# Performance work log

Hardware: AMD Instinct MI355X
Metric: run time of the kernel (lower is better)

Reference implementation:

```python
import jax, jax.numpy as jnp
import numpy as np

B, CIN, CE, CA, N, S = 2, 64, 128, 128, 1024, 32
SCALE = np.sqrt(np.float32(CA))  # scale_mode == 'dimfts'


def _vnlin(W, x):
    # VNLinear: linear map over the channel dim of (B, C, 3, N, S)
    return jnp.einsum('oc,bcdns->bodns', W, x)


def setup_inputs() -> dict:
    key = jax.random.key(0)
    ks = jax.random.split(key, 16)
    def w(k, o, i):
        return (jax.random.normal(k, (o, i), jnp.float32) / np.sqrt(np.float32(i)))
    return {
        'group_xyz': jax.random.normal(ks[0], (B, N, S, 3), jnp.float32),
        'group_fts': jax.random.normal(ks[1], (B, CIN, 3, N, S), jnp.float32),
        'query_xyz': jax.random.normal(ks[2], (B, N, 3), jnp.float32),
        'W_e1': w(ks[3], CE, CIN), 'W_e2': w(ks[4], CE, CE),
        'W_q': w(ks[5], CA, CE), 'W_k': w(ks[6], CA, CE), 'W_v': w(ks[7], CA, CE),
        'W_r1': w(ks[8], 64, 1), 'W_r2': w(ks[9], CA, 64),
        'W_std': w(ks[10], 3, CA),
        'W_f1': w(ks[11], CA, CA * 3), 'b_f1': jax.random.normal(ks[12], (CA,), jnp.float32) * 0.02,
        'W_f2': w(ks[13], CA, CA), 'b_f2': jax.random.normal(ks[14], (CA,), jnp.float32) * 0.02,
    }


def reference(group_xyz, group_fts, query_xyz, W_e1, W_e2, W_q, W_k, W_v,
              W_r1, W_r2, W_std, W_f1, b_f1, W_f2, b_f2):
    # vnn_e: two stacked VNLinear layers
    group_emb = _vnlin(W_e2, _vnlin(W_e1, group_fts))        # (B, CE, 3, N, S)
    query_emb = group_emb[..., :1]                           # (B, CE, 3, N, 1)
    q = _vnlin(W_q, query_emb)                               # (B, CA, 3, N, 1)
    k = _vnlin(W_k, group_emb)                               # (B, CA, 3, N, S)
    v = _vnlin(W_v, group_emb)                               # (B, CA, 3, N, S)

    # positional relation: xyz_rel -> (B, 1, 3, N, S) -> vnn_r
    xyz_rel = group_xyz - query_xyz[:, :, None, :]           # (B, N, S, 3)
    xyz_rel = jnp.transpose(xyz_rel[:, :, :, None, :], (0, 3, 4, 1, 2))  # (B,1,3,N,S)
    pos_rel = _vnlin(W_r2, _vnlin(W_r1, xyz_rel))            # (B, CA, 3, N, S)

    # relation_func == 'sub'
    attn = q - k + pos_rel                                   # (B, CA, 3, N, S)

    # VNStdFeatureLin (dim=5, no frame normalization): z0 = VNLinear(CA->3)
    z0 = _vnlin(W_std, attn)                                 # (B, 3, 3, N, S)
    attn = jnp.einsum('bijns,bjkns->bikns', attn, z0)        # (B, CA, 3, N, S) invariant

    # attn_fwd: 1x1 conv -> ReLU -> 1x1 conv on (B, CA*3, N, S)
    attn = attn.reshape(B, CA * 3, N, S)
    h = jax.nn.relu(jnp.einsum('oc,bcns->bons', W_f1, attn) + b_f1[:, None, None])
    a = jnp.einsum('oc,bcns->bons', W_f2, h) + b_f2[:, None, None]  # (B, CA, N, S)

    a = jax.nn.softmax(a[:, :, None, :, :] / SCALE, axis=-1)  # (B, CA, 1, N, S)
    v = v + pos_rel
    resi = jnp.sum(a * v, axis=-1)                            # (B, CA, 3, N)
    return resi
```

## Files before the change

kernel.cpp:

```cpp
#include <hip/hip_runtime.h>
#include <hip/hip_bf16.h>
#include <math.h>

typedef __hip_bfloat16  bf16;
typedef __hip_bfloat162 bf162;
typedef __attribute__((ext_vector_type(8))) short short8;
typedef __attribute__((ext_vector_type(4))) float f32x4;

#define BB   2
#define CINC 64
#define NN   1024
#define SSS  32
#define NS   (NN * SSS)

#define OFF_QT   0
#define OFF_WR   8192
#define OFF_WE21 8320
#define OFF_KB   16512
#define OFF_VB   20608
#define OFF_F1B  24704
#define OFF_F2B  49280
#define WS_NEED_FLOATS 57472

#define S_ATT_B 0
#define S_FTS_B 26112
#define S_SCR_B 26112
#define S_Q_B   39936
#define S_XYZ_B 40704
#define SMEM_BYTES 40896

__device__ __forceinline__ float bf2f(short s) {
    unsigned int u = ((unsigned int)(unsigned short)s) << 16;
    return __uint_as_float(u);
}
__device__ __forceinline__ short f2bf(float f) {
    bf16 h = __float2bfloat16(f);
    return *reinterpret_cast<short*>(&h);
}
__device__ __forceinline__ unsigned pk2(float a, float b) {
    bf162 p = __float22bfloat162_rn(make_float2(a, b));
    return *reinterpret_cast<unsigned*>(&p);
}

__global__ __launch_bounds__(256) void prep1(const float* __restrict__ We1,
                                             const float* __restrict__ We2,
                                             float* __restrict__ ws) {
    int e = blockIdx.x * 256 + threadIdx.x;
    int o = e >> 6, c = e & 63;
    float acc = 0.f;
    for (int m = 0; m < 128; ++m)
        acc = fmaf(We2[o * 128 + m], We1[m * 64 + c], acc);
    ws[OFF_WE21 + o * 64 + c] = acc;
}

__global__ __launch_bounds__(256) void prep2(const float* __restrict__ Wq,
                                             const float* __restrict__ Wk,
                                             const float* __restrict__ Wv,
                                             const float* __restrict__ Wr1,
                                             const float* __restrict__ Wr2,
                                             const float* __restrict__ Wf1,
                                             const float* __restrict__ Wf2,
                                             float* __restrict__ ws) {
    const float* we21 = ws + OFF_WE21;
    int e = blockIdx.x * 256 + threadIdx.x;
    if (e < 8192) {
        int i = e >> 6, c = e & 63;
        float acc = 0.f;
        for (int o = 0; o < 128; ++o)
            acc = fmaf(Wq[i * 128 + o], we21[o * 64 + c], acc);
        ws[OFF_QT + c * 128 + i] = acc;
    } else if (e < 24576) {
        int le = e - 8192;
        const float* W = (le < 8192) ? Wk : Wv;
        bf16* dst = (bf16*)(ws + ((le < 8192) ? OFF_KB : OFF_VB));
        int li = le & 8191;
        int i = li >> 6, c = li & 63;
        float acc = 0.f;
        for (int o = 0; o < 128; ++o)
            acc = fmaf(W[i * 128 + o], we21[o * 64 + c], acc);
        dst[i * 64 + c] = __float2bfloat16(acc);
    } else if (e < 24704) {
        int i = e - 24576;
        float acc = 0.f;
        for (int m = 0; m < 64; ++m)
            acc = fmaf(Wr2[i * 64 + m], Wr1[m], acc);
        ws[OFF_WR + i] = acc;
    } else if (e < 24704 + 49152) {
        int f = e - 24704;
        int o = f / 384, kp = f - o * 384;
        int c = (kp & 127) * 3 + (kp >> 7);
        ((bf16*)(ws + OFF_F1B))[f] = __float2bfloat16(Wf1[o * 384 + c]);
    } else if (e < 24704 + 49152 + 16384) {
        int f = e - (24704 + 49152);
        ((bf16*)(ws + OFF_F2B))[f] = __float2bfloat16(Wf2[f]);
    }
}

__global__ __launch_bounds__(256, 2) void fused_main(
        const float* __restrict__ gxyz, const float* __restrict__ gfts,
        const float* __restrict__ qxyz, const float* __restrict__ Wstd,
        const float* __restrict__ bf1,  const float* __restrict__ bf2,
        const float* __restrict__ ws,   float* __restrict__ out) {
    extern __shared__ char smc[];
    short* s_att  = (short*)(smc + S_ATT_B);
    short* h_t    = s_att;
    short* a_t    = s_att + 4352;
    short* fts_s  = (short*)(smc + S_FTS_B);
    float* s_scr  = (float*)(smc + S_SCR_B);
    short* s_qh   = (short*)(smc + S_Q_B);
    short* s_xyzh = (short*)(smc + S_XYZ_B);

    const int t    = threadIdx.x;
    const int bid  = blockIdx.x;
    const int b    = bid >> 10;
    const int n    = bid & 1023;
    const int w    = t >> 6;
    const int lane = t & 63;
    const int quad = lane >> 4;
    const int lq   = lane & 15;
    const int wb   = 32 * w;

    const float* gb = gfts + (size_t)b * (CINC * 3 * NS) + n * SSS;

    for (int l4 = t; l4 < 1536; l4 += 256) {
        int c  = l4 / 24;
        int m4 = (l4 - c * 24) * 4;
        int d  = m4 >> 5, s = m4 & 31;
        float4 f = *(const float4*)(gb + (c * 3 + d) * NS + s);
        fts_s[(m4 + 0) * 72 + c] = f2bf(f.x);
        fts_s[(m4 + 1) * 72 + c] = f2bf(f.y);
        fts_s[(m4 + 2) * 72 + c] = f2bf(f.z);
        fts_s[(m4 + 3) * 72 + c] = f2bf(f.w);
    }
    if (t >= 160) {
        int id = t - 160;
        int d = id >> 5, s = id & 31;
        s_xyzh[id] = f2bf(gxyz[((b * NN + n) * SSS + s) * 3 + d]
                          - qxyz[(b * NN + n) * 3 + d]);
    }
    __syncthreads();

    if (t < 128) {
        const float* qtw = ws + OFF_QT;
        float q0 = 0.f, q1 = 0.f, q2 = 0.f;
        for (int c = 0; c < 64; ++c) {
            float wq = qtw[c * 128 + t];
            q0 = fmaf(wq, bf2f(fts_s[c]),           q0);
            q1 = fmaf(wq, bf2f(fts_s[32 * 72 + c]), q1);
            q2 = fmaf(wq, bf2f(fts_s[64 * 72 + c]), q2);
        }
        s_qh[t * 3 + 0] = f2bf(q0);
        s_qh[t * 3 + 1] = f2bf(q1);
        s_qh[t * 3 + 2] = f2bf(q2);
    }
    __syncthreads();

    f32x4 va[6][2];
    {
        const short* kb = (const short*)(ws + OFF_KB);
        const short* vb = (const short*)(ws + OFF_VB);
        short8 Bk[2][2], Bv[2][2];
        #pragma unroll
        for (int it = 0; it < 2; ++it) {
            int irow = (wb + it * 16 + lq) * 64 + quad * 8;
            Bk[it][0] = *(const short8*)(kb + irow);
            Bk[it][1] = *(const short8*)(kb + irow + 32);
            Bv[it][0] = *(const short8*)(vb + irow);
            Bv[it][1] = *(const short8*)(vb + irow + 32);
        }
        float wr2[2] = { ws[OFF_WR + wb + lq], ws[OFF_WR + wb + 16 + lq] };
        #pragma unroll
        for (int mt = 0; mt < 6; ++mt) {
            const short* ap = fts_s + (mt * 16 + lq) * 72 + quad * 8;
            short8 A0 = *(const short8*)(ap);
            short8 A1 = *(const short8*)(ap + 32);
            int d = mt >> 1;
            #pragma unroll
            for (int it = 0; it < 2; ++it) {
                f32x4 kk = {0.f, 0.f, 0.f, 0.f};
                kk = __builtin_amdgcn_mfma_f32_16x16x32_bf16(A0, Bk[it][0], kk, 0, 0, 0);
                kk = __builtin_amdgcn_mfma_f32_16x16x32_bf16(A1, Bk[it][1], kk, 0, 0, 0);
                f32x4 vv = {0.f, 0.f, 0.f, 0.f};
                vv = __builtin_amdgcn_mfma_f32_16x16x32_bf16(A0, Bv[it][0], vv, 0, 0, 0);
                vv = __builtin_amdgcn_mfma_f32_16x16x32_bf16(A1, Bv[it][1], vv, 0, 0, 0);
                int i = wb + it * 16 + lq;
                float qd = bf2f(s_qh[i * 3 + d]);
                #pragma unroll
                for (int reg = 0; reg < 4; ++reg) {
                    int m = mt * 16 + quad * 4 + reg;
                    float pos = wr2[it] * bf2f(s_xyzh[m]);
                    s_att[m * 136 + i] = f2bf(qd - kk[reg] + pos);
                    va[mt][it][reg] = vv[reg] + pos;
                }
            }
        }
    }
    __syncthreads();

    {
        short8 As[4];
        #pragma unroll
        for (int kc = 0; kc < 4; ++kc) {
            short8 a = {0, 0, 0, 0, 0, 0, 0, 0};
            if (lq < 3) {
                const float* wp = Wstd + lq * 128 + kc * 32 + quad * 8;
                float4 w0 = *(const float4*)(wp);
                float4 w1 = *(const float4*)(wp + 4);
                a[0] = f2bf(w0.x); a[1] = f2bf(w0.y); a[2] = f2bf(w0.z); a[3] = f2bf(w0.w);
                a[4] = f2bf(w1.x); a[5] = f2bf(w1.y); a[6] = f2bf(w1.z); a[7] = f2bf(w1.w);
            }
            As[kc] = a;
        }
        for (int tile = w; tile < 6; tile += 4) {
            f32x4 acc = {0.f, 0.f, 0.f, 0.f};
            const short* bp = s_att + (tile * 16 + lq) * 136 + quad * 8;
            #pragma unroll
            for (int kc = 0; kc < 4; ++kc) {
                short8 bfr = *(const short8*)(bp + kc * 32);
                acc = __builtin_amdgcn_mfma_f32_16x16x32_bf16(As[kc], bfr, acc, 0, 0, 0);
            }
            if (quad == 0) {
                #pragma unroll
                for (int reg = 0; reg < 3; ++reg)
                    s_scr[reg * 96 + tile * 16 + lq] = acc[reg];
            }
        }
    }
    __syncthreads();

    for (int u = t; u < 512; u += 256) {
        int s  = u >> 4;
        int i0 = (u & 15) * 8;
        float z[3][3];
        #pragma unroll
        for (int j = 0; j < 3; ++j)
            #pragma unroll
            for (int kk = 0; kk < 3; ++kk)
                z[j][kk] = s_scr[j * 96 + kk * 32 + s];
        float af[3][8];
        #pragma unroll
        for (int j = 0; j < 3; ++j) {
            short8 v8 = *(const short8*)(s_att + (j * 32 + s) * 136 + i0);
            #pragma unroll
            for (int x = 0; x < 8; ++x) af[j][x] = bf2f(v8[x]);
        }
        #pragma unroll
        for (int kk = 0; kk < 3; ++kk) {
            short8 o8;
            #pragma unroll
            for (int x = 0; x < 8; ++x)
                o8[x] = f2bf(af[0][x] * z[0][kk] + af[1][x] * z[1][kk] + af[2][x] * z[2][kk]);
            *(short8*)(s_att + (kk * 32 + s) * 136 + i0) = o8;
        }
    }
    __syncthreads();

    f32x4 eacc[2][2];
    {
        f32x4 zz = {0.f, 0.f, 0.f, 0.f};
        eacc[0][0] = zz; eacc[0][1] = zz; eacc[1][0] = zz; eacc[1][1] = zz;
        const short* f1b = (const short*)(ws + OFF_F1B);
        const short* ab0 = f1b + (wb + lq) * 384 + quad * 8;
        const short* ab1 = ab0 + 16 * 384;
        #pragma unroll 2
        for (int ks = 0; ks < 12; ++ks) {
            int kk = ks >> 2;
            int ic = (ks & 3) * 32 + quad * 8;
            short8 a0 = *(const short8*)(ab0 + ks * 32);
            short8 a1 = *(const short8*)(ab1 + ks * 32);
            const short* bp = s_att + (kk * 32) * 136 + ic;
            short8 b0 = *(const short8*)(bp + lq * 136);
            short8 b1 = *(const short8*)(bp + (lq + 16) * 136);
            eacc[0][0] = __builtin_amdgcn_mfma_f32_16x16x32_bf16(a0, b0, eacc[0][0], 0, 0, 0);
            eacc[0][1] = __builtin_amdgcn_mfma_f32_16x16x32_bf16(a0, b1, eacc[0][1], 0, 0, 0);
            eacc[1][0] = __builtin_amdgcn_mfma_f32_16x16x32_bf16(a1, b0, eacc[1][0], 0, 0, 0);
            eacc[1][1] = __builtin_amdgcn_mfma_f32_16x16x32_bf16(a1, b1, eacc[1][1], 0, 0, 0);
        }
    }
    __syncthreads();

    #pragma unroll
    for (int mt = 0; mt < 2; ++mt) {
        int ob = wb + mt * 16 + quad * 4;
        float4 bb = *(const float4*)(bf1 + ob);
        float bv[4] = {bb.x, bb.y, bb.z, bb.w};
        #pragma unroll
        for (int nt = 0; nt < 2; ++nt) {
            f32x4 c = eacc[mt][nt];
            int s = nt * 16 + lq;
            uint2 pk;
            pk.x = pk2(fmaxf(c[0] + bv[0], 0.f), fmaxf(c[1] + bv[1], 0.f));
            pk.y = pk2(fmaxf(c[2] + bv[2], 0.f), fmaxf(c[3] + bv[3], 0.f));
            *(uint2*)(h_t + s * 136 + ob) = pk;
        }
    }
    __syncthreads();

    {
        f32x4 facc[2][2];
        f32x4 zz = {0.f, 0.f, 0.f, 0.f};
        facc[0][0] = zz; facc[0][1] = zz; facc[1][0] = zz; facc[1][1] = zz;
        const short* f2b = (const short*)(ws + OFF_F2B);
        const short* ab0 = f2b + (wb + lq) * 128 + quad * 8;
        const short* ab1 = ab0 + 16 * 128;
        #pragma unroll 2
        for (int ks = 0; ks < 4; ++ks) {
            int c0 = ks * 32 + quad * 8;
            short8 a0 = *(const short8*)(ab0 + ks * 32);
            short8 a1 = *(const short8*)(ab1 + ks * 32);
            short8 b0 = *(const short8*)(h_t + lq * 136 + c0);
            short8 b1 = *(const short8*)(h_t + (lq + 16) * 136 + c0);
            facc[0][0] = __builtin_amdgcn_mfma_f32_16x16x32_bf16(a0, b0, facc[0][0], 0, 0, 0);
            facc[0][1] = __builtin_amdgcn_mfma_f32_16x16x32_bf16(a0, b1, facc[0][1], 0, 0, 0);
            facc[1][0] = __builtin_amdgcn_mfma_f32_16x16x32_bf16(a1, b0, facc[1][0], 0, 0, 0);
            facc[1][1] = __builtin_amdgcn_mfma_f32_16x16x32_bf16(a1, b1, facc[1][1], 0, 0, 0);
        }
        #pragma unroll
        for (int mt = 0; mt < 2; ++mt) {
            int ob = wb + mt * 16 + quad * 4;
            float4 bb = *(const float4*)(bf2 + ob);
            float bv[4] = {bb.x, bb.y, bb.z, bb.w};
            #pragma unroll
            for (int nt = 0; nt < 2; ++nt) {
                f32x4 c = facc[mt][nt];
                int s = nt * 16 + lq;
                uint2 pk;
                pk.x = pk2(c[0] + bv[0], c[1] + bv[1]);
                pk.y = pk2(c[2] + bv[2], c[3] + bv[3]);
                *(uint2*)(a_t + s * 136 + ob) = pk;
            }
        }
    }
    __syncthreads();

    if (t < 128) {
        float vals[32];
        #pragma unroll
        for (int s = 0; s < 32; ++s) vals[s] = bf2f(a_t[s * 136 + t]);
        float mx = -INFINITY;
        #pragma unroll
        for (int s = 0; s < 32; ++s) mx = fmaxf(mx, vals[s]);
        const float inv = 0.08838834764831845f;
        float sum = 0.f;
        #pragma unroll
        for (int s = 0; s < 32; ++s) { vals[s] = __expf((vals[s] - mx) * inv); sum += vals[s]; }
        float rs = 1.f / sum;
        #pragma unroll
        for (int s = 0; s < 32; ++s) a_t[s * 136 + t] = f2bf(vals[s] * rs);
    }
    __syncthreads();

    {
        float pr[2][3];
        #pragma unroll
        for (int it = 0; it < 2; ++it)
            #pragma unroll
            for (int d = 0; d < 3; ++d) pr[it][d] = 0.f;
        #pragma unroll
        for (int mt = 0; mt < 6; ++mt) {
            int d = mt >> 1;
            #pragma unroll
            for (int it = 0; it < 2; ++it) {
                int i = wb + it * 16 + lq;
                #pragma unroll
                for (int reg = 0; reg < 4; ++reg) {
                    int s = (mt & 1) * 16 + quad * 4 + reg;
                    pr[it][d] = fmaf(bf2f(a_t[s * 136 + i]), va[mt][it][reg], pr[it][d]);
                }
            }
        }
        #pragma unroll
        for (int it = 0; it < 2; ++it)
            #pragma unroll
            for (int d = 0; d < 3; ++d) {
                float v = pr[it][d];
                v += __shfl_xor(v, 16);
                v += __shfl_xor(v, 32);
                if (quad == 0) s_scr[(wb + it * 16 + lq) * 3 + d] = v;
            }
    }
    __syncthreads();

    for (int e = t; e < 384; e += 256)
        out[(b * 384 + e) * NN + n] = s_scr[e];
}

extern "C" void kernel_launch(void* const* d_in, const int* in_sizes, int n_in,
                              void* d_out, int out_size, void* d_ws, size_t ws_size,
                              hipStream_t stream) {
    const float* gxyz = (const float*)d_in[0];
    const float* gfts = (const float*)d_in[1];
    const float* qxyz = (const float*)d_in[2];
    const float* We1  = (const float*)d_in[3];
    const float* We2  = (const float*)d_in[4];
    const float* Wq   = (const float*)d_in[5];
    const float* Wk   = (const float*)d_in[6];
    const float* Wv   = (const float*)d_in[7];
    const float* Wr1  = (const float*)d_in[8];
    const float* Wr2  = (const float*)d_in[9];
    const float* Wstd = (const float*)d_in[10];
    const float* bf1  = (const float*)d_in[12];
    const float* bf2  = (const float*)d_in[14];
    float* out = (float*)d_out;
    float* ws  = (float*)d_ws;

    (void)hipFuncSetAttribute((const void*)fused_main,
                              hipFuncAttributeMaxDynamicSharedMemorySize, SMEM_BYTES);

    prep1<<<32, 256, 0, stream>>>(We1, We2, ws);
    prep2<<<353, 256, 0, stream>>>(Wq, Wk, Wv, Wr1, Wr2,
                                   (const float*)d_in[11], (const float*)d_in[13], ws);
    fused_main<<<BB * NN, 256, SMEM_BYTES, stream>>>(gxyz, gfts, qxyz, Wstd,
                                                     bf1, bf2, ws, out);
}
```

Baseline: 188.9 us.

## Fold query projection into K MFMA, stage features in halves, pack V in bf16

The separate scalar q-projection pass and its barrier are removed. The query term is folded into the K MFMA through a concatenated [Wk | -Wq] weight, using broadcast query-row A operands, which adds two MFMAs per tile. The input features are loaded and converted in two halves, reusing a smaller fts buffer, so shared memory drops. The v+pos accumulators are packed to bf16 to cut register pressure, at some precision cost and with an extra barrier per half.

Result: no change. 189.5 us (+0.3%).

```diff
diff --git a/kernel.cpp b/kernel.cpp
--- a/kernel.cpp
+++ b/kernel.cpp
@@ -13,21 +13,20 @@
 #define SSS  32
 #define NS   (NN * SSS)
 
-#define OFF_QT   0
+#define OFF_WE21 0
 #define OFF_WR   8192
-#define OFF_WE21 8320
-#define OFF_KB   16512
-#define OFF_VB   20608
-#define OFF_F1B  24704
-#define OFF_F2B  49280
-#define WS_NEED_FLOATS 57472
-
-#define S_ATT_B 0
-#define S_FTS_B 26112
-#define S_SCR_B 26112
-#define S_Q_B   39936
-#define S_XYZ_B 40704
-#define SMEM_BYTES 40896
+#define OFF_KBA  8320
+#define OFF_VB   16512
+#define OFF_F1B  20608
+#define OFF_F2B  45184
+#define WS_NEED_FLOATS 53376
+
+#define S_ATT_B  0
+#define S_FTS_B  26112
+#define S_SCR_B  26112
+#define S_QSRC_B 33024
+#define S_XYZ_B  33184
+#define SMEM_BYTES 33408
 
 __device__ __forceinline__ float bf2f(short s) {
     unsigned int u = ((unsigned int)(unsigned short)s) << 16;
@@ -63,22 +62,22 @@
                                              float* __restrict__ ws) {
     const float* we21 = ws + OFF_WE21;
     int e = blockIdx.x * 256 + threadIdx.x;
-    if (e < 8192) {
-        int i = e >> 6, c = e & 63;
-        float acc = 0.f;
-        for (int o = 0; o < 128; ++o)
-            acc = fmaf(Wq[i * 128 + o], we21[o * 64 + c], acc);
-        ws[OFF_QT + c * 128 + i] = acc;
-    } else if (e < 24576) {
-        int le = e - 8192;
-        const float* W = (le < 8192) ? Wk : Wv;
-        bf16* dst = (bf16*)(ws + ((le < 8192) ? OFF_KB : OFF_VB));
-        int li = le & 8191;
-        int i = li >> 6, c = li & 63;
+    if (e < 16384) {
+        int i = e >> 7, c2 = e & 127;
+        const float* W = (c2 < 64) ? Wk : Wq;
+        int c = c2 & 63;
         float acc = 0.f;
         for (int o = 0; o < 128; ++o)
             acc = fmaf(W[i * 128 + o], we21[o * 64 + c], acc);
-        dst[i * 64 + c] = __float2bfloat16(acc);
+        if (c2 >= 64) acc = -acc;
+        ((bf16*)(ws + OFF_KBA))[i * 128 + c2] = __float2bfloat16(acc);
+    } else if (e < 24576) {
+        int le = e - 16384;
+        int i = le >> 6, c = le & 63;
+        float acc = 0.f;
+        for (int o = 0; o < 128; ++o)
+            acc = fmaf(Wv[i * 128 + o], we21[o * 64 + c], acc);
+        ((bf16*)(ws + OFF_VB))[i * 64 + c] = __float2bfloat16(acc);
     } else if (e < 24704) {
         int i = e - 24576;
         float acc = 0.f;
@@ -107,7 +106,7 @@
     short* a_t    = s_att + 4352;
     short* fts_s  = (short*)(smc + S_FTS_B);
     float* s_scr  = (float*)(smc + S_SCR_B);
-    short* s_qh   = (short*)(smc + S_Q_B);
+    short* q_src  = (short*)(smc + S_QSRC_B);
     short* s_xyzh = (short*)(smc + S_XYZ_B);
 
     const int t    = threadIdx.x;
@@ -122,80 +121,85 @@
 
     const float* gb = gfts + (size_t)b * (CINC * 3 * NS) + n * SSS;
 
-    for (int l4 = t; l4 < 1536; l4 += 256) {
-        int c  = l4 / 24;
-        int m4 = (l4 - c * 24) * 4;
-        int d  = m4 >> 5, s = m4 & 31;
-        float4 f = *(const float4*)(gb + (c * 3 + d) * NS + s);
-        fts_s[(m4 + 0) * 72 + c] = f2bf(f.x);
-        fts_s[(m4 + 1) * 72 + c] = f2bf(f.y);
-        fts_s[(m4 + 2) * 72 + c] = f2bf(f.z);
-        fts_s[(m4 + 3) * 72 + c] = f2bf(f.w);
-    }
-    if (t >= 160) {
-        int id = t - 160;
-        int d = id >> 5, s = id & 31;
-        s_xyzh[id] = f2bf(gxyz[((b * NN + n) * SSS + s) * 3 + d]
-                          - qxyz[(b * NN + n) * 3 + d]);
-    }
-    __syncthreads();
-
-    if (t < 128) {
-        const float* qtw = ws + OFF_QT;
-        float q0 = 0.f, q1 = 0.f, q2 = 0.f;
-        for (int c = 0; c < 64; ++c) {
-            float wq = qtw[c * 128 + t];
-            q0 = fmaf(wq, bf2f(fts_s[c]),           q0);
-            q1 = fmaf(wq, bf2f(fts_s[32 * 72 + c]), q1);
-            q2 = fmaf(wq, bf2f(fts_s[64 * 72 + c]), q2);
-        }
-        s_qh[t * 3 + 0] = f2bf(q0);
-        s_qh[t * 3 + 1] = f2bf(q1);
-        s_qh[t * 3 + 2] = f2bf(q2);
-    }
-    __syncthreads();
-
-    f32x4 va[6][2];
+    short8 Ka[2][4], Va[2][2];
     {
-        const short* kb = (const short*)(ws + OFF_KB);
-        const short* vb = (const short*)(ws + OFF_VB);
-        short8 Bk[2][2], Bv[2][2];
+        const short* kba = (const short*)(ws + OFF_KBA);
+        const short* vbb = (const short*)(ws + OFF_VB);
         #pragma unroll
         for (int it = 0; it < 2; ++it) {
-            int irow = (wb + it * 16 + lq) * 64 + quad * 8;
-            Bk[it][0] = *(const short8*)(kb + irow);
-            Bk[it][1] = *(const short8*)(kb + irow + 32);
-            Bv[it][0] = *(const short8*)(vb + irow);
-            Bv[it][1] = *(const short8*)(vb + irow + 32);
-        }
-        float wr2[2] = { ws[OFF_WR + wb + lq], ws[OFF_WR + wb + 16 + lq] };
-        #pragma unroll
-        for (int mt = 0; mt < 6; ++mt) {
-            const short* ap = fts_s + (mt * 16 + lq) * 72 + quad * 8;
-            short8 A0 = *(const short8*)(ap);
-            short8 A1 = *(const short8*)(ap + 32);
-            int d = mt >> 1;
+            int i = wb + it * 16 + lq;
+            #pragma unroll
+            for (int kc = 0; kc < 4; ++kc)
+                Ka[it][kc] = *(const short8*)(kba + i * 128 + kc * 32 + quad * 8);
+            #pragma unroll
+            for (int kc = 0; kc < 2; ++kc)
+                Va[it][kc] = *(const short8*)(vbb + i * 64 + kc * 32 + quad * 8);
+        }
+    }
+    float wr2[2] = { ws[OFF_WR + wb + lq], ws[OFF_WR + wb + 16 + lq] };
+
+    uint2 va_pk[6][2];
+    #pragma unroll
+    for (int h = 0; h < 2; ++h) {
+        for (int l4 = t; l4 < 768; l4 += 256) {
+            int c  = l4 / 12;
+            int mq = l4 - c * 12;
+            int ml = mq * 4;
+            int mg = h * 48 + ml;
+            int d  = mg >> 5, s = mg & 31;
+            float4 f = *(const float4*)(gb + (c * 3 + d) * NS + s);
+            fts_s[(ml + 0) * 72 + c] = f2bf(f.x);
+            fts_s[(ml + 1) * 72 + c] = f2bf(f.y);
+            fts_s[(ml + 2) * 72 + c] = f2bf(f.z);
+            fts_s[(ml + 3) * 72 + c] = f2bf(f.w);
+            if (h == 0 && ml == 32) q_src[c] = f2bf(f.x);
+        }
+        if (h == 0 && t >= 160) {
+            int id = t - 160;
+            int d = id >> 5, s = id & 31;
+            s_xyzh[id] = f2bf(gxyz[((b * NN + n) * SSS + s) * 3 + d]
+                              - qxyz[(b * NN + n) * 3 + d]);
+        }
+        __syncthreads();
+
+        #pragma unroll
+        for (int mt_h = 0; mt_h < 3; ++mt_h) {
+            int mt = h * 3 + mt_h;
+            int d  = mt >> 1;
+            const short* ap = fts_s + (mt_h * 16 + lq) * 72 + quad * 8;
+            short8 a0 = *(const short8*)(ap);
+            short8 a1 = *(const short8*)(ap + 32);
+            const short* qp;
+            if (h == 0) qp = fts_s + (d * 32) * 72 + quad * 8;
+            else        qp = (d == 1) ? (q_src + quad * 8)
+                                      : (fts_s + 16 * 72 + quad * 8);
+            short8 aq0 = *(const short8*)(qp);
+            short8 aq1 = *(const short8*)(qp + 32);
             #pragma unroll
             for (int it = 0; it < 2; ++it) {
                 f32x4 kk = {0.f, 0.f, 0.f, 0.f};
-                kk = __builtin_amdgcn_mfma_f32_16x16x32_bf16(A0, Bk[it][0], kk, 0, 0, 0);
-                kk = __builtin_amdgcn_mfma_f32_16x16x32_bf16(A1, Bk[it][1], kk, 0, 0, 0);
+                kk = __builtin_amdgcn_mfma_f32_16x16x32_bf16(a0,  Ka[it][0], kk, 0, 0, 0);
+                kk = __builtin_amdgcn_mfma_f32_16x16x32_bf16(a1,  Ka[it][1], kk, 0, 0, 0);
+                kk = __builtin_amdgcn_mfma_f32_16x16x32_bf16(aq0, Ka[it][2], kk, 0, 0, 0);
+                kk = __builtin_amdgcn_mfma_f32_16x16x32_bf16(aq1, Ka[it][3], kk, 0, 0, 0);
                 f32x4 vv = {0.f, 0.f, 0.f, 0.f};
-                vv = __builtin_amdgcn_mfma_f32_16x16x32_bf16(A0, Bv[it][0], vv, 0, 0, 0);
-                vv = __builtin_amdgcn_mfma_f32_16x16x32_bf16(A1, Bv[it][1], vv, 0, 0, 0);
+                vv = __builtin_amdgcn_mfma_f32_16x16x32_bf16(a0,  Va[it][0], vv, 0, 0, 0);
+                vv = __builtin_amdgcn_mfma_f32_16x16x32_bf16(a1,  Va[it][1], vv, 0, 0, 0);
                 int i = wb + it * 16 + lq;
-                float qd = bf2f(s_qh[i * 3 + d]);
+                float p[4];
                 #pragma unroll
                 for (int reg = 0; reg < 4; ++reg) {
                     int m = mt * 16 + quad * 4 + reg;
                     float pos = wr2[it] * bf2f(s_xyzh[m]);
-                    s_att[m * 136 + i] = f2bf(qd - kk[reg] + pos);
-                    va[mt][it][reg] = vv[reg] + pos;
+                    s_att[m * 136 + i] = f2bf(pos - kk[reg]);
+                    p[reg] = vv[reg] + pos;
                 }
-            }
-        }
-    }
-    __syncthreads();
+                va_pk[mt][it].x = pk2(p[0], p[1]);
+                va_pk[mt][it].y = pk2(p[2], p[3]);
+            }
+        }
+        __syncthreads();
+    }
 
     {
         short8 As[4];
@@ -359,14 +363,19 @@
         #pragma unroll
         for (int mt = 0; mt < 6; ++mt) {
             int d = mt >> 1;
+            int s0 = (mt & 1) * 16 + quad * 4;
             #pragma unroll
             for (int it = 0; it < 2; ++it) {
                 int i = wb + it * 16 + lq;
-                #pragma unroll
-                for (int reg = 0; reg < 4; ++reg) {
-                    int s = (mt & 1) * 16 + quad * 4 + reg;
-                    pr[it][d] = fmaf(bf2f(a_t[s * 136 + i]), va[mt][it][reg], pr[it][d]);
-                }
+                uint2 vp = va_pk[mt][it];
+                float v0 = bf2f((short)(vp.x & 0xffff));
+                float v1 = bf2f((short)(vp.x >> 16));
+                float v2 = bf2f((short)(vp.y & 0xffff));
+                float v3 = bf2f((short)(vp.y >> 16));
+                pr[it][d] = fmaf(bf2f(a_t[(s0 + 0) * 136 + i]), v0, pr[it][d]);
+                pr[it][d] = fmaf(bf2f(a_t[(s0 + 1) * 136 + i]), v1, pr[it][d]);
+                pr[it][d] = fmaf(bf2f(a_t[(s0 + 2) * 136 + i]), v2, pr[it][d]);
+                pr[it][d] = fmaf(bf2f(a_t[(s0 + 3) * 136 + i]), v3, pr[it][d]);
             }
         }
         #pragma unroll
```
